# Kernel tuning notes

Hardware: AMD Instinct MI355X
Metric: run time of the kernel (lower is better)

The kernel has to match this reference:

```python
import jax, jax.numpy as jnp
import numpy as np


def setup_inputs() -> dict:
    key = jax.random.key(0)
    k1, k2 = jax.random.split(key)
    inputs = jax.random.normal(k1, (32768, 512), dtype=jnp.float32)
    codebook = jax.random.normal(k2, (8192, 512), dtype=jnp.float32)
    return {"inputs": inputs, "codebook": codebook}


def reference(inputs, codebook):
    # inputs: [N, D] (flattened), codebook: [K, D]
    D = codebook.shape[1]
    x = inputs.reshape(-1, D)                          # [N, D]
    cb_sqr = jnp.sum(codebook ** 2, axis=1)            # [K]
    x_sqr = jnp.sum(x ** 2, axis=1, keepdims=True)     # [N, 1]
    distances = (cb_sqr[None, :] + x_sqr) - 2.0 * jnp.einsum('nd,kd->nk', x, codebook)
    soft_distances = jax.nn.softmax(-distances, axis=1)  # [N, K]
    return soft_distances
```

## Files before the change

### kernel.cpp

```cpp
#include <hip/hip_runtime.h>


typedef __attribute__((ext_vector_type(8))) __bf16 bf16x8;
typedef __attribute__((ext_vector_type(4))) float f32x4;

typedef __attribute__((address_space(1))) const void global_cvoid;
typedef __attribute__((address_space(3))) void lds_void;

__device__ inline unsigned short f32_to_bf16_rne(float f) {
    unsigned int u = __float_as_uint(f);
    unsigned int r = u + 0x7FFFu + ((u >> 16) & 1u);
    return (unsigned short)(r >> 16);
}
__device__ inline float bf16u_to_f32(unsigned short h) {
    return __uint_as_float(((unsigned int)h) << 16);
}

__global__ void split_kernel(const float* __restrict__ in,
                             unsigned short* __restrict__ hi,
                             unsigned short* __restrict__ lo, int n4) {
    int i = blockIdx.x * blockDim.x + threadIdx.x;
    int stride = gridDim.x * blockDim.x;
    for (; i < n4; i += stride) {
        float4 v = reinterpret_cast<const float4*>(in)[i];
        float vv[4] = {v.x, v.y, v.z, v.w};
        ushort4 hv, lv;
        unsigned short h[4], l[4];
#pragma unroll
        for (int j = 0; j < 4; ++j) {
            h[j] = f32_to_bf16_rne(vv[j]);
            float r = vv[j] - bf16u_to_f32(h[j]);
            l[j] = f32_to_bf16_rne(r);
        }
        hv.x = h[0]; hv.y = h[1]; hv.z = h[2]; hv.w = h[3];
        lv.x = l[0]; lv.y = l[1]; lv.z = l[2]; lv.w = l[3];
        reinterpret_cast<ushort4*>(hi)[i] = hv;
        reinterpret_cast<ushort4*>(lo)[i] = lv;
    }
}

__global__ void rowsq_kernel(const float* __restrict__ cb, float* __restrict__ out) {
    int row = blockIdx.x * 4 + (threadIdx.x >> 6);
    int lane = threadIdx.x & 63;
    const float4* p = reinterpret_cast<const float4*>(cb + (size_t)row * 512);
    float4 a = p[lane];
    float4 b = p[lane + 64];
    float s = a.x * a.x + a.y * a.y + a.z * a.z + a.w * a.w +
              b.x * b.x + b.y * b.y + b.z * b.z + b.w * b.w;
#pragma unroll
    for (int o = 32; o >= 1; o >>= 1) s += __shfl_xor(s, o);
    if (lane == 0) out[row] = s;
}


#define ST_ALL(tt_, b_)                                                                 \
    { int prod_ = (tt_) >> 3, ch_ = (tt_) & 7;                                          \
      const unsigned short* Abase_ = (prod_ < 2 ? Ah : Al) + arow0 + ch_ * 64;          \
      const unsigned short* Bbase_ = (prod_ == 1 ? Bl : Bh) + brow0 + ch_ * 64;         \
      _Pragma("unroll") for (int kk_ = 0; kk_ < 2; ++kk_) {                             \
        _Pragma("unroll") for (int j = 0; j < 2; ++j) {                                 \
          __builtin_amdgcn_global_load_lds((global_cvoid*)(Abase_ + kk_ * 32 + goff[j]),\
              (lds_void*)&lds[b_][0][kk_][sl8[j]], 16, 0, 0);                           \
          __builtin_amdgcn_global_load_lds((global_cvoid*)(Bbase_ + kk_ * 32 + goff[j]),\
              (lds_void*)&lds[b_][1][kk_][sl8[j]], 16, 0, 0);                           \
        } } }

template <int F16>
__global__ __launch_bounds__(512, 2) void gemm_kernel(
    const unsigned short* __restrict__ Ah, const unsigned short* __restrict__ Al,
    const unsigned short* __restrict__ Bh, const unsigned short* __restrict__ Bl,
    const float* __restrict__ cbq, float* __restrict__ outf,
    unsigned short* __restrict__ p16, float* __restrict__ max_part,
    float* __restrict__ sum_part) {
    __shared__ __align__(16) unsigned short lds[2][2][2][8192];

    const int t = threadIdx.x;
    const int lane = t & 63;
    const int w = t >> 6;
    const int wm = w >> 2, wn = w & 3;
    const int fr = lane & 15, fg = lane >> 4;

    int bid = blockIdx.x;
    int swz = (bid & 7) * 512 + (bid >> 3);
    const int bm = swz >> 5, bn = swz & 31;
    const int row0 = bm * 256, col0 = bn * 256;
    const size_t arow0 = (size_t)row0 * 512;
    const size_t brow0 = (size_t)col0 * 512;

    const int xsl = fg ^ ((fr >> 2) & 3);
    const int a_slot = (wm * 128 + fr) * 4 + xsl;
    const int b_slot = (wn * 64 + fr) * 4 + xsl;

    int goff[2], sl8[2];
#pragma unroll
    for (int j = 0; j < 2; ++j) {
        int s = j * 512 + t;
        int r_ = s >> 2, cp_ = s & 3;
        int cl_ = cp_ ^ ((r_ >> 2) & 3);
        goff[j] = r_ * 512 + cl_ * 8;
        sl8[j] = s * 8;
    }

    f32x4 acc[8][4] = {};

    ST_ALL(0, 0);

    for (int tt = 0; tt < 24; ++tt) {
        const int cur = tt & 1;
        __builtin_amdgcn_sched_barrier(0);
        __builtin_amdgcn_s_barrier();
        __builtin_amdgcn_sched_barrier(0);
        if (tt < 23) {
            ST_ALL(tt + 1, cur ^ 1);
            asm volatile("s_waitcnt vmcnt(8)" ::: "memory");
        } else {
            asm volatile("s_waitcnt vmcnt(0)" ::: "memory");
        }
        __builtin_amdgcn_sched_barrier(0);
        __builtin_amdgcn_s_barrier();
        __builtin_amdgcn_sched_barrier(0);
#pragma unroll
        for (int kk = 0; kk < 2; ++kk) {
            bf16x8 bfr[4], afrA[4], afrB[4];
#pragma unroll
            for (int n = 0; n < 4; ++n)
                bfr[n] = *(const bf16x8*)&lds[cur][1][kk][(b_slot + n * 64) * 8];
#pragma unroll
            for (int m = 0; m < 4; ++m)
                afrA[m] = *(const bf16x8*)&lds[cur][0][kk][(a_slot + m * 64) * 8];
#pragma unroll
            for (int m = 0; m < 4; ++m)
                afrB[m] = *(const bf16x8*)&lds[cur][0][kk][(a_slot + (m + 4) * 64) * 8];
#pragma unroll
            for (int m = 0; m < 4; ++m)
#pragma unroll
                for (int n = 0; n < 4; ++n)
                    acc[m][n] = __builtin_amdgcn_mfma_f32_16x16x32_bf16(
                        afrA[m], bfr[n], acc[m][n], 0, 0, 0);
#pragma unroll
            for (int m = 0; m < 4; ++m)
#pragma unroll
                for (int n = 0; n < 4; ++n)
                    acc[4 + m][n] = __builtin_amdgcn_mfma_f32_16x16x32_bf16(
                        afrB[m], bfr[n], acc[4 + m][n], 0, 0, 0);
        }
    }

    float* redm = (float*)&lds[0][0][0][0];
    float* reds = redm + 1024;

    float cq[4];
#pragma unroll
    for (int n = 0; n < 4; ++n) cq[n] = cbq[col0 + wn * 64 + n * 16 + fr];
#pragma unroll
    for (int m = 0; m < 8; ++m)
#pragma unroll
        for (int n = 0; n < 4; ++n)
#pragma unroll
            for (int r = 0; r < 4; ++r)
                acc[m][n][r] = 2.0f * acc[m][n][r] - cq[n];

    float rmx[8][4];
#pragma unroll
    for (int m = 0; m < 8; ++m)
#pragma unroll
        for (int r = 0; r < 4; ++r) {
            float v = fmaxf(fmaxf(acc[m][0][r], acc[m][1][r]),
                            fmaxf(acc[m][2][r], acc[m][3][r]));
#pragma unroll
            for (int o = 1; o < 16; o <<= 1) v = fmaxf(v, __shfl_xor(v, o));
            rmx[m][r] = v;
        }
    __syncthreads();
    if (fr == 0) {
#pragma unroll
        for (int m = 0; m < 8; ++m)
#pragma unroll
            for (int r = 0; r < 4; ++r)
                redm[wn * 256 + wm * 128 + m * 16 + fg * 4 + r] = rmx[m][r];
    }
    __syncthreads();
#pragma unroll
    for (int m = 0; m < 8; ++m)
#pragma unroll
        for (int r = 0; r < 4; ++r) {
            int row = wm * 128 + m * 16 + fg * 4 + r;
            rmx[m][r] = fmaxf(fmaxf(redm[row], redm[256 + row]),
                              fmaxf(redm[512 + row], redm[768 + row]));
        }
#pragma unroll
    for (int m = 0; m < 8; ++m)
#pragma unroll
        for (int r = 0; r < 4; ++r) {
            float s = 0.f;
#pragma unroll
            for (int n = 0; n < 4; ++n) s += __expf(acc[m][n][r] - rmx[m][r]);
#pragma unroll
            for (int o = 1; o < 16; o <<= 1) s += __shfl_xor(s, o);
            if (fr == 0) reds[wn * 256 + wm * 128 + m * 16 + fg * 4 + r] = s;
        }
    __syncthreads();
    if (wn == 0 && fr == 0) {
#pragma unroll
        for (int m = 0; m < 8; ++m)
#pragma unroll
            for (int r = 0; r < 4; ++r) {
                int row = wm * 128 + m * 16 + fg * 4 + r;
                size_t gr = (size_t)(row0 + row);
                max_part[gr * 32 + bn] = rmx[m][r];
                sum_part[gr * 32 + bn] =
                    reds[row] + reds[256 + row] + reds[512 + row] + reds[768 + row];
            }
    }
#pragma unroll
    for (int m = 0; m < 8; ++m)
#pragma unroll
        for (int n = 0; n < 4; ++n)
#pragma unroll
            for (int r = 0; r < 4; ++r) {
                size_t gr = (size_t)(row0 + wm * 128 + m * 16 + fg * 4 + r);
                size_t gi = gr * 8192 + col0 + wn * 64 + n * 16 + fr;
                if constexpr (F16) {
                    union { _Float16 h; unsigned short u; } cv;
                    cv.h = (_Float16)__expf(acc[m][n][r] - rmx[m][r]);
                    p16[gi] = cv.u;
                } else {
                    outf[gi] = acc[m][n][r];
                }
            }
}

__global__ void combine_kernel(const float* __restrict__ max_part,
                               const float* __restrict__ sum_part,
                               float* __restrict__ row_m, float* __restrict__ row_is,
                               float* __restrict__ scale, int do_scale) {
    int row = blockIdx.x * 8 + (threadIdx.x >> 5);
    int l = threadIdx.x & 31;
    size_t off = (size_t)row * 32 + l;
    float m = max_part[off];
    float s = sum_part[off];
    float gm = m;
#pragma unroll
    for (int o = 16; o >= 1; o >>= 1) gm = fmaxf(gm, __shfl_xor(gm, o, 32));
    float c = s * __expf(m - gm);
#pragma unroll
    for (int o = 16; o >= 1; o >>= 1) c += __shfl_xor(c, o, 32);
    float inv = 1.0f / c;
    if (do_scale) scale[off] = __expf(m - gm) * inv;
    if (l == 0) {
        row_m[row] = gm;
        row_is[row] = inv;
    }
}

__global__ void norm_kernel(float* __restrict__ out, const float* __restrict__ row_m,
                            const float* __restrict__ row_is) {
    size_t i = (size_t)blockIdx.x * blockDim.x + threadIdx.x;
    size_t stride = (size_t)gridDim.x * blockDim.x;
    const size_t n4 = 268435456ull / 4;
    float4* p = reinterpret_cast<float4*>(out);
    for (; i < n4; i += stride) {
        int row = (int)(i >> 11);
        float m = row_m[row];
        float is = row_is[row];
        float4 v = p[i];
        v.x = __expf(v.x - m) * is;
        v.y = __expf(v.y - m) * is;
        v.z = __expf(v.z - m) * is;
        v.w = __expf(v.w - m) * is;
        p[i] = v;
    }
}

__global__ void norm_f16_kernel(const unsigned short* __restrict__ p16,
                                const float* __restrict__ scale,
                                float* __restrict__ out) {
    size_t i = (size_t)blockIdx.x * blockDim.x + threadIdx.x;
    size_t stride = (size_t)gridDim.x * blockDim.x;
    const size_t ng = 268435456ull / 8;
    const uint4* src = reinterpret_cast<const uint4*>(p16);
    float4* dst = reinterpret_cast<float4*>(out);
    for (; i < ng; i += stride) {
        int row = (int)(i >> 10);
        int bn = (int)((i >> 5) & 31);
        float s = scale[(size_t)row * 32 + bn];
        union { uint4 u; _Float16 h[8]; } cv;
        cv.u = src[i];
        float4 o1, o2;
        o1.x = (float)cv.h[0] * s; o1.y = (float)cv.h[1] * s;
        o1.z = (float)cv.h[2] * s; o1.w = (float)cv.h[3] * s;
        o2.x = (float)cv.h[4] * s; o2.y = (float)cv.h[5] * s;
        o2.z = (float)cv.h[6] * s; o2.w = (float)cv.h[7] * s;
        dst[i * 2] = o1;
        dst[i * 2 + 1] = o2;
    }
}

extern "C" void kernel_launch(void* const* d_in, const int* in_sizes, int n_in,
                              void* d_out, int out_size, void* d_ws, size_t ws_size,
                              hipStream_t stream) {
    const float* x = (const float*)d_in[0];
    const float* cb = (const float*)d_in[1];
    float* out = (float*)d_out;
    char* ws = (char*)d_ws;

    unsigned short* Xh = (unsigned short*)(ws);
    unsigned short* Xl = (unsigned short*)(ws + 33554432ull);
    unsigned short* Ch = (unsigned short*)(ws + 67108864ull);
    unsigned short* Cl = (unsigned short*)(ws + 75497472ull);
    float* cbq       = (float*)(ws + 83886080ull);
    float* max_part  = (float*)(ws + 83918848ull);
    float* sum_part  = (float*)(ws + 88113152ull);
    float* row_m     = (float*)(ws + 92307456ull);
    float* row_is    = (float*)(ws + 92438528ull);
    float* scale     = (float*)(ws + 92569600ull);
    unsigned short* p16 = (unsigned short*)(ws + 96763904ull);

    const bool f16path = (ws_size >= 633634816ull);

    split_kernel<<<2048, 256, 0, stream>>>(x, Xh, Xl, 32768 * 512 / 4);
    split_kernel<<<1024, 256, 0, stream>>>(cb, Ch, Cl, 8192 * 512 / 4);
    rowsq_kernel<<<2048, 256, 0, stream>>>(cb, cbq);
    if (f16path) {
        gemm_kernel<1><<<4096, 512, 0, stream>>>(Xh, Xl, Ch, Cl, cbq, out, p16,
                                                 max_part, sum_part);
        combine_kernel<<<4096, 256, 0, stream>>>(max_part, sum_part, row_m, row_is,
                                                 scale, 1);
        norm_f16_kernel<<<4096, 256, 0, stream>>>(p16, scale, out);
    } else {
        gemm_kernel<0><<<4096, 512, 0, stream>>>(Xh, Xl, Ch, Cl, cbq, out, p16,
                                                 max_part, sum_part);
        combine_kernel<<<4096, 256, 0, stream>>>(max_part, sum_part, row_m, row_is,
                                                 scale, 0);
        norm_kernel<<<4096, 256, 0, stream>>>(out, row_m, row_is);
    }
}
```

Measured before the change: 1.602 ms.

## Interleave LDS reads, async global-to-LDS loads and MFMA in finer-grained phases

Splits each k-tile iteration into four phases. Each phase reads A/B fragments from LDS, issues one slice of the next tile's global_load_lds prefetch, and runs a 4x4 MFMA block at raised wave priority (s_setprio). Partial vmcnt waits with barriers replace the single bulk prefetch-then-wait, so memory traffic overlaps compute more evenly and register use for fragments drops. In exchange it adds more barriers per iteration, and the hand-tuned waitcnt counts carry a risk of synchronisation hazards.

```diff
diff --git a/kernel.cpp b/kernel.cpp
--- a/kernel.cpp
+++ b/kernel.cpp
@@ -53,17 +53,34 @@
 }
 
 
-#define ST_ALL(tt_, b_)                                                                 \
-    { int prod_ = (tt_) >> 3, ch_ = (tt_) & 7;                                          \
-      const unsigned short* Abase_ = (prod_ < 2 ? Ah : Al) + arow0 + ch_ * 64;          \
-      const unsigned short* Bbase_ = (prod_ == 1 ? Bl : Bh) + brow0 + ch_ * 64;         \
-      _Pragma("unroll") for (int kk_ = 0; kk_ < 2; ++kk_) {                             \
-        _Pragma("unroll") for (int j = 0; j < 2; ++j) {                                 \
-          __builtin_amdgcn_global_load_lds((global_cvoid*)(Abase_ + kk_ * 32 + goff[j]),\
-              (lds_void*)&lds[b_][0][kk_][sl8[j]], 16, 0, 0);                           \
-          __builtin_amdgcn_global_load_lds((global_cvoid*)(Bbase_ + kk_ * 32 + goff[j]),\
-              (lds_void*)&lds[b_][1][kk_][sl8[j]], 16, 0, 0);                           \
-        } } }
+#define RD_A(mq_, kk_, b_)                                                        \
+    { _Pragma("unroll") for (int m = 0; m < 4; ++m)                               \
+        afr[m] = *(const bf16x8*)&lds[b_][0][kk_][(a_slot + ((mq_)*4 + m) * 64) * 8]; }
+
+#define RD_B(kk_, b_)                                                             \
+    { _Pragma("unroll") for (int n = 0; n < 4; ++n)                               \
+        bfr[n] = *(const bf16x8*)&lds[b_][1][kk_][(b_slot + n * 64) * 8]; }
+
+#define ST(mat_, kk_, b_, tt_)                                                    \
+    { int prod_ = (tt_) >> 3, ch_ = (tt_) & 7;                                    \
+      const unsigned short* bse_;                                                 \
+      if ((mat_) == 0) bse_ = (prod_ < 2 ? Ah : Al) + arow0;                      \
+      else             bse_ = (prod_ == 1 ? Bl : Bh) + brow0;                     \
+      bse_ += ch_ * 64 + (kk_) * 32;                                              \
+      _Pragma("unroll") for (int j = 0; j < 2; ++j)                               \
+          __builtin_amdgcn_global_load_lds((global_cvoid*)(bse_ + goff[j]),       \
+              (lds_void*)&lds[b_][mat_][kk_][sl8[j]], 16, 0, 0);                  \
+    }
+
+#define MM(mq_)                                                                   \
+    { _Pragma("unroll") for (int m = 0; m < 4; ++m)                               \
+      _Pragma("unroll") for (int n = 0; n < 4; ++n)                               \
+          acc[(mq_) * 4 + m][n] = __builtin_amdgcn_mfma_f32_16x16x32_bf16(        \
+              afr[m], bfr[n], acc[(mq_) * 4 + m][n], 0, 0, 0); }
+
+#define MIDSYNC()                                                                 \
+    { __builtin_amdgcn_s_barrier();                                               \
+      asm volatile("s_waitcnt lgkmcnt(0)" ::: "memory"); }
 
 template <int F16>
 __global__ __launch_bounds__(512, 2) void gemm_kernel(
@@ -102,47 +119,46 @@
     }
 
     f32x4 acc[8][4] = {};
-
-    ST_ALL(0, 0);
+    bf16x8 afr[4], bfr[4];
+
+    ST(0, 0, 0, 0);
+    ST(1, 0, 0, 0);
+    ST(0, 1, 0, 0);
+    ST(1, 1, 0, 0);
+    asm volatile("s_waitcnt vmcnt(4)\n\ts_barrier" ::: "memory");
 
     for (int tt = 0; tt < 24; ++tt) {
-        const int cur = tt & 1;
-        __builtin_amdgcn_sched_barrier(0);
+        const int cur = tt & 1, nb = cur ^ 1;
+        const bool pf = (tt < 23);
+        RD_B(0, cur);
+        RD_A(0, 0, cur);
+        if (pf) ST(0, 0, nb, tt + 1);
+        MIDSYNC();
+        __builtin_amdgcn_s_setprio(1); MM(0); __builtin_amdgcn_s_setprio(0);
         __builtin_amdgcn_s_barrier();
-        __builtin_amdgcn_sched_barrier(0);
-        if (tt < 23) {
-            ST_ALL(tt + 1, cur ^ 1);
-            asm volatile("s_waitcnt vmcnt(8)" ::: "memory");
+        RD_A(1, 0, cur);
+        if (pf) ST(1, 0, nb, tt + 1);
+        MIDSYNC();
+        __builtin_amdgcn_s_setprio(1); MM(1); __builtin_amdgcn_s_setprio(0);
+        if (pf) {
+            asm volatile("s_waitcnt vmcnt(4)\n\ts_barrier" ::: "memory");
         } else {
-            asm volatile("s_waitcnt vmcnt(0)" ::: "memory");
-        }
-        __builtin_amdgcn_sched_barrier(0);
+            asm volatile("s_waitcnt vmcnt(0)\n\ts_barrier" ::: "memory");
+        }
+        RD_B(1, cur);
+        RD_A(0, 1, cur);
+        if (pf) ST(0, 1, nb, tt + 1);
+        MIDSYNC();
+        __builtin_amdgcn_s_setprio(1); MM(0); __builtin_amdgcn_s_setprio(0);
         __builtin_amdgcn_s_barrier();
-        __builtin_amdgcn_sched_barrier(0);
-#pragma unroll
-        for (int kk = 0; kk < 2; ++kk) {
-            bf16x8 bfr[4], afrA[4], afrB[4];
-#pragma unroll
-            for (int n = 0; n < 4; ++n)
-                bfr[n] = *(const bf16x8*)&lds[cur][1][kk][(b_slot + n * 64) * 8];
-#pragma unroll
-            for (int m = 0; m < 4; ++m)
-                afrA[m] = *(const bf16x8*)&lds[cur][0][kk][(a_slot + m * 64) * 8];
-#pragma unroll
-            for (int m = 0; m < 4; ++m)
-                afrB[m] = *(const bf16x8*)&lds[cur][0][kk][(a_slot + (m + 4) * 64) * 8];
-#pragma unroll
-            for (int m = 0; m < 4; ++m)
-#pragma unroll
-                for (int n = 0; n < 4; ++n)
-                    acc[m][n] = __builtin_amdgcn_mfma_f32_16x16x32_bf16(
-                        afrA[m], bfr[n], acc[m][n], 0, 0, 0);
-#pragma unroll
-            for (int m = 0; m < 4; ++m)
-#pragma unroll
-                for (int n = 0; n < 4; ++n)
-                    acc[4 + m][n] = __builtin_amdgcn_mfma_f32_16x16x32_bf16(
-                        afrB[m], bfr[n], acc[4 + m][n], 0, 0, 0);
+        RD_A(1, 1, cur);
+        if (pf) ST(1, 1, nb, tt + 1);
+        MIDSYNC();
+        __builtin_amdgcn_s_setprio(1); MM(1); __builtin_amdgcn_s_setprio(0);
+        if (pf) {
+            asm volatile("s_waitcnt vmcnt(4)\n\ts_barrier" ::: "memory");
+        } else {
+            __builtin_amdgcn_s_barrier();
         }
     }
 
```

After: 1.406 ms. 1.14x faster.
